# Kernel optimization log

Hardware: AMD Instinct MI355X
Metric: run time of the kernel (lower is better)

## Reference

```python
import jax, jax.numpy as jnp
import numpy as np

EPS = 1e-10


def setup_inputs() -> dict:
    key = jax.random.key(0)
    k1, k2 = jax.random.split(key)
    B, C, H, W = 8, 16, 256, 256
    x = jax.random.normal(k1, (B, C, H, W), dtype=jnp.float32)
    # grid_sample-style normalized coords in [-1, 1]
    inv_grid = jax.random.uniform(k2, (B, H, W, 2), dtype=jnp.float32, minval=-1.0, maxval=1.0)
    return {"x": x, "inv_grid": inv_grid}


def reference(x, inv_grid):
    B, C, Hin, Win = x.shape
    h, w = Hin, Win  # OH = OW = None -> output size equals input size

    g = (inv_grid + 1.0) * 0.5
    # coord 0 scaled by h, coord 1 by w, shifted by +1 (padding row/col), clamped
    ci = jnp.clip(g[..., 0] * h + 1.0, 0.0, h + 1 - 2 * EPS)
    cj = jnp.clip(g[..., 1] * w + 1.0, 0.0, w + 1 - 2 * EPS)
    i0 = jnp.floor(ci).astype(jnp.int32)  # coords >= 0 so floor == trunc (.long())
    j0 = jnp.floor(cj).astype(jnp.int32)

    # broadcast over channel dim (grid is shared across channels)
    ci_ = ci[:, None]
    cj_ = cj[:, None]
    i0_ = i0[:, None]
    j0_ = j0[:, None]

    bidx = jnp.arange(B)[:, None, None, None]
    cidx = jnp.arange(C)[None, :, None, None]

    A = jnp.zeros((B, C, h + 3, w + 3), dtype=x.dtype)
    for di in range(2):
        wi = jax.nn.relu(1.0 - jnp.abs(ci_ - (i0_ + di).astype(ci_.dtype)))
        for dj in range(2):
            wj = jax.nn.relu(1.0 - jnp.abs(cj_ - (j0_ + dj).astype(cj_.dtype)))
            # bilinear splat scatter-add of x * weight into the 4 corner cells
            A = A.at[bidx, cidx, i0_ + di, j0_ + dj].add(x * (wi * wj))
    return A[..., 1:h + 1, 1:w + 1]
```

## Files before the change

kernel.cpp:

```cpp
#include <hip/hip_runtime.h>
#include <hip/hip_fp16.h>
#include <stdint.h>

#define BB 8
#define CC 16
#define HH 256
#define WW 256
#define HW (HH * WW)
#define NSRC (BB * HW)
#define NBLK (NSRC / 256)
#define REC_DW 9
#define ELLCAP 12
#define MAXSLOT 15
#define CNT_BYTES ((size_t)NSRC * 4)


__global__ __launch_bounds__(256) void pass1_ell(
    const float* __restrict__ x,
    const float* __restrict__ inv_grid,
    uint32_t* __restrict__ counts,
    uint32_t* __restrict__ records)
{
    const int idx = blockIdx.x * 256 + threadIdx.x;
    const float2 g2 = ((const float2*)inv_grid)[idx];

    const float ci = fminf(fmaxf(fmaf((g2.x + 1.0f) * 0.5f, (float)HH, 1.0f), 0.0f), 257.0f);
    const float cj = fminf(fmaxf(fmaf((g2.y + 1.0f) * 0.5f, (float)WW, 1.0f), 0.0f), 257.0f);
    const int i0 = (int)floorf(ci);
    const int j0 = (int)floorf(cj);
    const float fi = ci - (float)i0;
    const float fj = cj - (float)j0;

    const int bi = i0 - 1, bj = j0 - 1;
    if (!(((unsigned)bi < HH) & ((unsigned)bj < WW))) return;

    const int b = idx >> 16;
    const int p = idx & 0xFFFF;

    const float* xp = x + (((size_t)b * CC) << 16) + p;
    float xv[CC];
#pragma unroll
    for (int q = 0; q < CC; ++q) xv[q] = xp[(size_t)q << 16];

    const uint32_t bin = (b << 16) | (bi << 8) | bj;
    const uint32_t slot = atomicAdd(&counts[bin], 1u);
    if (slot >= ELLCAP) return;

    uint32_t* rp = records + ((size_t)bin * ELLCAP + slot) * REC_DW;
    const uint32_t fi16 = (uint32_t)(fi * 65535.0f + 0.5f);
    const uint32_t fj16 = (uint32_t)(fj * 65535.0f + 0.5f);
    rp[0] = fi16 | (fj16 << 16);
#pragma unroll
    for (int q = 0; q < 8; ++q) {
        const uint32_t h0 = (uint32_t)__half_as_ushort(__float2half_rn(xv[2 * q]));
        const uint32_t h1 = (uint32_t)__half_as_ushort(__float2half_rn(xv[2 * q + 1]));
        rp[1 + q] = h0 | (h1 << 16);
    }
}

__global__ __launch_bounds__(256) void gather_ell(
    const uint32_t* __restrict__ counts,
    const uint32_t* __restrict__ records,
    float* __restrict__ out)
{
    const int g   = blockIdx.x;
    const int b   = g & 7;
    const int seq = g >> 3;
    const int r   = ((seq >> 4) << 4) + (threadIdx.x >> 4);
    const int c   = ((seq & 15) << 4) + (threadIdx.x & 15);

    float acc[CC];
#pragma unroll
    for (int q = 0; q < CC; ++q) acc[q] = 0.0f;

#pragma unroll
    for (int di = 0; di < 2; ++di) {
        const int i0c = r + di;
        if (i0c < 1) continue;
#pragma unroll
        for (int dj = 0; dj < 2; ++dj) {
            const int j0c = c + dj;
            if (j0c < 1) continue;
            const uint32_t bin = (b << 16) | ((i0c - 1) << 8) | (j0c - 1);
            uint32_t cnt = counts[bin];
            if (cnt > ELLCAP) cnt = ELLCAP;
            const uint32_t* rp = records + (size_t)bin * (ELLCAP * REC_DW);
            for (uint32_t k = 0; k < cnt; ++k, rp += REC_DW) {
                const uint32_t ff = rp[0];
                const float fi = (float)(ff & 0xFFFFu) * (1.0f / 65535.0f);
                const float fj = (float)(ff >> 16)     * (1.0f / 65535.0f);
                const float wi = di ? (1.0f - fi) : fi;
                const float wj = dj ? (1.0f - fj) : fj;
                const float w = wi * wj;
#pragma unroll
                for (int q = 0; q < 8; ++q) {
                    const uint32_t u = rp[1 + q];
                    const float v0 = __half2float(__ushort_as_half((unsigned short)(u & 0xFFFFu)));
                    const float v1 = __half2float(__ushort_as_half((unsigned short)(u >> 16)));
                    acc[2 * q]     += w * v0;
                    acc[2 * q + 1] += w * v1;
                }
            }
        }
    }

    float* op = out + (((size_t)(b * CC)) << 16) + (r << 8) + c;
#pragma unroll
    for (int q = 0; q < CC; ++q)
        op[(size_t)q << 16] = acc[q];
}

__global__ __launch_bounds__(256) void pass1_bin(
    const float* __restrict__ inv_grid,
    uint32_t* __restrict__ counts,
    uint32_t* __restrict__ srcmeta,
    uint32_t* __restrict__ fifj)
{
    const int idx = blockIdx.x * 256 + threadIdx.x;
    const float2 g2 = ((const float2*)inv_grid)[idx];
    const float ci = fminf(fmaxf(fmaf((g2.x + 1.0f) * 0.5f, (float)HH, 1.0f), 0.0f), 257.0f);
    const float cj = fminf(fmaxf(fmaf((g2.y + 1.0f) * 0.5f, (float)WW, 1.0f), 0.0f), 257.0f);
    const int i0 = (int)floorf(ci);
    const int j0 = (int)floorf(cj);
    const float fi = ci - (float)i0;
    const float fj = cj - (float)j0;
    const int bi = i0 - 1, bj = j0 - 1;
    uint32_t meta = 0xFFFFFFFFu;
    if (((unsigned)bi < HH) & ((unsigned)bj < WW)) {
        const int b = idx >> 16;
        const uint32_t bin = (b << 16) | (bi << 8) | bj;
        const uint32_t slot = atomicAdd(&counts[bin], 1u);
        if (slot < MAXSLOT) meta = (bin << 4) | slot;
    }
    srcmeta[idx] = meta;
    const uint32_t fi16 = (uint32_t)(fi * 65535.0f + 0.5f);
    const uint32_t fj16 = (uint32_t)(fj * 65535.0f + 0.5f);
    fifj[idx] = fi16 | (fj16 << 16);
}

__global__ __launch_bounds__(256) void scanA(
    const uint32_t* __restrict__ counts,
    uint32_t* __restrict__ offsets,
    uint32_t* __restrict__ bsum)
{
    __shared__ uint32_t s[256];
    const int t = threadIdx.x;
    const int i = blockIdx.x * 256 + t;
    const uint32_t v = counts[i];
    s[t] = v;
    __syncthreads();
#pragma unroll
    for (int d = 1; d < 256; d <<= 1) {
        const uint32_t u = (t >= d) ? s[t - d] : 0u;
        __syncthreads();
        s[t] += u;
        __syncthreads();
    }
    offsets[i] = s[t] - v;
    if (t == 255) bsum[blockIdx.x] = s[255];
}

__global__ __launch_bounds__(1024) void scanB(uint32_t* __restrict__ bsum)
{
    __shared__ uint32_t s[1024];
    const int t = threadIdx.x;
    const uint32_t a  = bsum[2 * t];
    const uint32_t b2 = bsum[2 * t + 1];
    const uint32_t pair = a + b2;
    s[t] = pair;
    __syncthreads();
#pragma unroll
    for (int d = 1; d < 1024; d <<= 1) {
        const uint32_t u = (t >= d) ? s[t - d] : 0u;
        __syncthreads();
        s[t] += u;
        __syncthreads();
    }
    const uint32_t excl = s[t] - pair;
    bsum[2 * t]     = excl;
    bsum[2 * t + 1] = excl + a;
}

__global__ __launch_bounds__(256) void fill_records(
    const float* __restrict__ x,
    const uint32_t* __restrict__ srcmeta,
    const uint32_t* __restrict__ fifj,
    const uint32_t* __restrict__ offsets,
    const uint32_t* __restrict__ bsum,
    uint32_t* __restrict__ records)
{
    const int idx = blockIdx.x * 256 + threadIdx.x;
    const uint32_t meta = srcmeta[idx];
    if (meta == 0xFFFFFFFFu) return;
    const uint32_t bin  = meta >> 4;
    const uint32_t slot = meta & 15u;
    const uint32_t pos  = offsets[bin] + bsum[bin >> 8] + slot;
    const int b = idx >> 16;
    const int p = idx & 0xFFFF;
    const float* xp = x + (((size_t)b * CC) << 16) + p;
    uint32_t* rp = records + (size_t)pos * REC_DW;
    rp[0] = fifj[idx];
#pragma unroll
    for (int q = 0; q < 8; ++q) {
        const float v0 = xp[(size_t)(2 * q)     << 16];
        const float v1 = xp[(size_t)(2 * q + 1) << 16];
        const uint32_t h0 = (uint32_t)__half_as_ushort(__float2half_rn(v0));
        const uint32_t h1 = (uint32_t)__half_as_ushort(__float2half_rn(v1));
        rp[1 + q] = h0 | (h1 << 16);
    }
}

__global__ __launch_bounds__(256) void gather_csr(
    const uint32_t* __restrict__ counts,
    const uint32_t* __restrict__ offsets,
    const uint32_t* __restrict__ bsum,
    const uint32_t* __restrict__ records,
    float* __restrict__ out)
{
    const int g   = blockIdx.x;
    const int b   = g & 7;
    const int seq = g >> 3;
    const int r   = ((seq >> 4) << 4) + (threadIdx.x >> 4);
    const int c   = ((seq & 15) << 4) + (threadIdx.x & 15);

    float acc[CC];
#pragma unroll
    for (int q = 0; q < CC; ++q) acc[q] = 0.0f;

#pragma unroll
    for (int di = 0; di < 2; ++di) {
        const int i0c = r + di;
        if (i0c < 1) continue;
#pragma unroll
        for (int dj = 0; dj < 2; ++dj) {
            const int j0c = c + dj;
            if (j0c < 1) continue;
            const uint32_t bin = (b << 16) | ((i0c - 1) << 8) | (j0c - 1);
            uint32_t cnt = counts[bin];
            if (cnt > MAXSLOT) cnt = MAXSLOT;
            const uint32_t off = offsets[bin] + bsum[bin >> 8];
            const uint32_t* rp = records + (size_t)off * REC_DW;
            for (uint32_t k = 0; k < cnt; ++k, rp += REC_DW) {
                const uint32_t ff = rp[0];
                const float fi = (float)(ff & 0xFFFFu) * (1.0f / 65535.0f);
                const float fj = (float)(ff >> 16)     * (1.0f / 65535.0f);
                const float wi = di ? (1.0f - fi) : fi;
                const float wj = dj ? (1.0f - fj) : fj;
                const float w = wi * wj;
#pragma unroll
                for (int q = 0; q < 8; ++q) {
                    const uint32_t u = rp[1 + q];
                    const float v0 = __half2float(__ushort_as_half((unsigned short)(u & 0xFFFFu)));
                    const float v1 = __half2float(__ushort_as_half((unsigned short)(u >> 16)));
                    acc[2 * q]     += w * v0;
                    acc[2 * q + 1] += w * v1;
                }
            }
        }
    }

    float* op = out + (((size_t)(b * CC)) << 16) + (r << 8) + c;
#pragma unroll
    for (int q = 0; q < CC; ++q)
        op[(size_t)q << 16] = acc[q];
}

__global__ __launch_bounds__(256) void invgrid_scatter_direct(
    const float* __restrict__ x,
    const float* __restrict__ inv_grid,
    float* __restrict__ out)
{
    const int idx = blockIdx.x * 256 + threadIdx.x;
    const int b = idx >> 16;
    const float2 g2 = ((const float2*)inv_grid)[idx];
    const float ci = fminf(fmaxf(fmaf((g2.x + 1.0f) * 0.5f, (float)HH, 1.0f), 0.0f), 257.0f);
    const float cj = fminf(fmaxf(fmaf((g2.y + 1.0f) * 0.5f, (float)WW, 1.0f), 0.0f), 257.0f);
    const int i0 = (int)floorf(ci);
    const int j0 = (int)floorf(cj);
    const float wi0 = fmaxf(0.0f, 1.0f - fabsf(ci - (float)i0));
    const float wi1 = fmaxf(0.0f, 1.0f - fabsf(ci - (float)(i0 + 1)));
    const float wj0 = fmaxf(0.0f, 1.0f - fabsf(cj - (float)j0));
    const float wj1 = fmaxf(0.0f, 1.0f - fabsf(cj - (float)(j0 + 1)));
    const float w00 = wi0 * wj0, w01 = wi0 * wj1;
    const float w10 = wi1 * wj0, w11 = wi1 * wj1;
    const int r0 = i0 - 1, r1 = i0, c0 = j0 - 1, c1 = j0;
    const bool vr0 = (unsigned)r0 < HH, vr1 = (unsigned)r1 < HH;
    const bool vc0 = (unsigned)c0 < WW, vc1 = (unsigned)c1 < WW;
    const int o00 = r0 * WW + c0, o01 = r0 * WW + c1;
    const int o10 = r1 * WW + c0, o11 = r1 * WW + c1;
    const int p = idx & 0xFFFF;
    const float* xp = x + (size_t)b * CC * HW + p;
    float* op = out + (size_t)b * CC * HW;
#pragma unroll
    for (int cch = 0; cch < CC; ++cch) {
        const float xv = xp[(size_t)cch * HW];
        float* ob = op + (size_t)cch * HW;
        if (vr0 & vc0) atomicAdd(ob + o00, xv * w00);
        if (vr0 & vc1) atomicAdd(ob + o01, xv * w01);
        if (vr1 & vc0) atomicAdd(ob + o10, xv * w10);
        if (vr1 & vc1) atomicAdd(ob + o11, xv * w11);
    }
}

extern "C" void kernel_launch(void* const* d_in, const int* in_sizes, int n_in,
                              void* d_out, int out_size, void* d_ws, size_t ws_size,
                              hipStream_t stream) {
    const float* x        = (const float*)d_in[0];
    const float* inv_grid = (const float*)d_in[1];
    float* out            = (float*)d_out;

    const size_t ell_need = CNT_BYTES + (size_t)NSRC * ELLCAP * REC_DW * 4;

    const size_t A = 256;
    size_t o_counts  = 0;
    size_t o_offsets = o_counts  + ((size_t)NSRC * 4 + A - 1) / A * A;
    size_t o_bsum    = o_offsets + ((size_t)NSRC * 4 + A - 1) / A * A;
    size_t o_srcmeta = o_bsum    + ((size_t)NBLK * 4 + A - 1) / A * A;
    size_t o_fifj    = o_srcmeta + ((size_t)NSRC * 4 + A - 1) / A * A;
    size_t o_records = o_fifj    + ((size_t)NSRC * 4 + A - 1) / A * A;
    size_t csr_need  = o_records + (size_t)NSRC * REC_DW * 4;

    if (ws_size >= ell_need) {
        uint32_t* counts  = (uint32_t*)d_ws;
        uint32_t* records = (uint32_t*)((char*)d_ws + CNT_BYTES);
        hipMemsetAsync(counts, 0, CNT_BYTES, stream);
        pass1_ell <<<NBLK, 256, 0, stream>>>(x, inv_grid, counts, records);
        gather_ell<<<NBLK, 256, 0, stream>>>(counts, records, out);
    } else if (ws_size >= csr_need) {
        char* w = (char*)d_ws;
        uint32_t* counts  = (uint32_t*)(w + o_counts);
        uint32_t* offsets = (uint32_t*)(w + o_offsets);
        uint32_t* bsum    = (uint32_t*)(w + o_bsum);
        uint32_t* srcmeta = (uint32_t*)(w + o_srcmeta);
        uint32_t* fifj    = (uint32_t*)(w + o_fifj);
        uint32_t* records = (uint32_t*)(w + o_records);
        hipMemsetAsync(counts, 0, (size_t)NSRC * 4, stream);
        pass1_bin   <<<NBLK, 256,  0, stream>>>(inv_grid, counts, srcmeta, fifj);
        scanA       <<<NBLK, 256,  0, stream>>>(counts, offsets, bsum);
        scanB       <<<1,    1024, 0, stream>>>(bsum);
        fill_records<<<NBLK, 256,  0, stream>>>(x, srcmeta, fifj, offsets, bsum, records);
        gather_csr  <<<NBLK, 256,  0, stream>>>(counts, offsets, bsum, records, out);
    } else {
        hipMemsetAsync(d_out, 0, (size_t)out_size * sizeof(float), stream);
        invgrid_scatter_direct<<<NBLK, 256, 0, stream>>>(x, inv_grid, out);
    }
}
```

Baseline: 165.3 us.

## Split ELL build into meta and fill passes with slot-major SoA records

Splits the first pass into a metadata kernel that does the atomic slot allocation and a separate fill kernel that reads x and writes fp16 payloads. Records move from an interleaved 9-dword layout to a slot-major structure-of-arrays: one array of packed weights and one of 32-byte payloads written as two uint4 stores. This is meant to give coalesced, vectorized stores in the fill step and coalesced loads in the gather, where neighbouring threads read neighbouring bins at the same slot. The cost is an extra kernel launch, an intermediate srcs buffer, and a larger workspace requirement. If the workspace is too small, execution falls back to the CSR path.

```diff
diff --git a/kernel.cpp b/kernel.cpp
--- a/kernel.cpp
+++ b/kernel.cpp
@@ -9,17 +9,16 @@
 #define HW (HH * WW)
 #define NSRC (BB * HW)
 #define NBLK (NSRC / 256)
-#define REC_DW 9
 #define ELLCAP 12
 #define MAXSLOT 15
+#define REC_DW 9
 #define CNT_BYTES ((size_t)NSRC * 4)
 
 
-__global__ __launch_bounds__(256) void pass1_ell(
-    const float* __restrict__ x,
+__global__ __launch_bounds__(256) void pass1_meta(
     const float* __restrict__ inv_grid,
     uint32_t* __restrict__ counts,
-    uint32_t* __restrict__ records)
+    uint2* __restrict__ srcs)
 {
     const int idx = blockIdx.x * 256 + threadIdx.x;
     const float2 g2 = ((const float2*)inv_grid)[idx];
@@ -32,35 +31,54 @@
     const float fj = cj - (float)j0;
 
     const int bi = i0 - 1, bj = j0 - 1;
-    if (!(((unsigned)bi < HH) & ((unsigned)bj < WW))) return;
+    uint32_t pos = 0xFFFFFFFFu;
+    if (((unsigned)bi < HH) & ((unsigned)bj < WW)) {
+        const int b = idx >> 16;
+        const uint32_t bin = (b << 16) | (bi << 8) | bj;
+        const uint32_t slot = atomicAdd(&counts[bin], 1u);
+        if (slot < ELLCAP) pos = slot * (uint32_t)NSRC + bin;
+    }
+    const uint32_t fi16 = (uint32_t)(fi * 65535.0f + 0.5f);
+    const uint32_t fj16 = (uint32_t)(fj * 65535.0f + 0.5f);
+    uint2 m; m.x = pos; m.y = fi16 | (fj16 << 16);
+    srcs[idx] = m;
+}
+
+__global__ __launch_bounds__(256) void fill_ell(
+    const float* __restrict__ x,
+    const uint2* __restrict__ srcs,
+    uint32_t* __restrict__ ff,
+    uint4* __restrict__ pl)
+{
+    const int idx = blockIdx.x * 256 + threadIdx.x;
+    const uint2 m = srcs[idx];
+    if (m.x == 0xFFFFFFFFu) return;
+    const uint32_t pos = m.x;
 
     const int b = idx >> 16;
     const int p = idx & 0xFFFF;
-
     const float* xp = x + (((size_t)b * CC) << 16) + p;
-    float xv[CC];
-#pragma unroll
-    for (int q = 0; q < CC; ++q) xv[q] = xp[(size_t)q << 16];
-
-    const uint32_t bin = (b << 16) | (bi << 8) | bj;
-    const uint32_t slot = atomicAdd(&counts[bin], 1u);
-    if (slot >= ELLCAP) return;
-
-    uint32_t* rp = records + ((size_t)bin * ELLCAP + slot) * REC_DW;
-    const uint32_t fi16 = (uint32_t)(fi * 65535.0f + 0.5f);
-    const uint32_t fj16 = (uint32_t)(fj * 65535.0f + 0.5f);
-    rp[0] = fi16 | (fj16 << 16);
+
+    uint32_t h[8];
 #pragma unroll
     for (int q = 0; q < 8; ++q) {
-        const uint32_t h0 = (uint32_t)__half_as_ushort(__float2half_rn(xv[2 * q]));
-        const uint32_t h1 = (uint32_t)__half_as_ushort(__float2half_rn(xv[2 * q + 1]));
-        rp[1 + q] = h0 | (h1 << 16);
-    }
+        const float v0 = xp[(size_t)(2 * q)     << 16];
+        const float v1 = xp[(size_t)(2 * q + 1) << 16];
+        const uint32_t h0 = (uint32_t)__half_as_ushort(__float2half_rn(v0));
+        const uint32_t h1 = (uint32_t)__half_as_ushort(__float2half_rn(v1));
+        h[q] = h0 | (h1 << 16);
+    }
+    ff[pos] = m.y;
+    uint4 q0; q0.x = h[0]; q0.y = h[1]; q0.z = h[2]; q0.w = h[3];
+    uint4 q1; q1.x = h[4]; q1.y = h[5]; q1.z = h[6]; q1.w = h[7];
+    pl[(size_t)pos * 2]     = q0;
+    pl[(size_t)pos * 2 + 1] = q1;
 }
 
 __global__ __launch_bounds__(256) void gather_ell(
     const uint32_t* __restrict__ counts,
-    const uint32_t* __restrict__ records,
+    const uint32_t* __restrict__ ff,
+    const uint4* __restrict__ pl,
     float* __restrict__ out)
 {
     const int g   = blockIdx.x;
@@ -84,19 +102,21 @@
             const uint32_t bin = (b << 16) | ((i0c - 1) << 8) | (j0c - 1);
             uint32_t cnt = counts[bin];
             if (cnt > ELLCAP) cnt = ELLCAP;
-            const uint32_t* rp = records + (size_t)bin * (ELLCAP * REC_DW);
-            for (uint32_t k = 0; k < cnt; ++k, rp += REC_DW) {
-                const uint32_t ff = rp[0];
-                const float fi = (float)(ff & 0xFFFFu) * (1.0f / 65535.0f);
-                const float fj = (float)(ff >> 16)     * (1.0f / 65535.0f);
+            for (uint32_t k = 0; k < cnt; ++k) {
+                const uint32_t pos = k * (uint32_t)NSRC + bin;
+                const uint32_t f2 = ff[pos];
+                const float fi = (float)(f2 & 0xFFFFu) * (1.0f / 65535.0f);
+                const float fj = (float)(f2 >> 16)     * (1.0f / 65535.0f);
                 const float wi = di ? (1.0f - fi) : fi;
                 const float wj = dj ? (1.0f - fj) : fj;
                 const float w = wi * wj;
+                const uint4 q0 = pl[(size_t)pos * 2];
+                const uint4 q1 = pl[(size_t)pos * 2 + 1];
+                const uint32_t hs[8] = {q0.x, q0.y, q0.z, q0.w, q1.x, q1.y, q1.z, q1.w};
 #pragma unroll
                 for (int q = 0; q < 8; ++q) {
-                    const uint32_t u = rp[1 + q];
-                    const float v0 = __half2float(__ushort_as_half((unsigned short)(u & 0xFFFFu)));
-                    const float v1 = __half2float(__ushort_as_half((unsigned short)(u >> 16)));
+                    const float v0 = __half2float(__ushort_as_half((unsigned short)(hs[q] & 0xFFFFu)));
+                    const float v1 = __half2float(__ushort_as_half((unsigned short)(hs[q] >> 16)));
                     acc[2 * q]     += w * v0;
                     acc[2 * q + 1] += w * v1;
                 }
@@ -241,9 +261,9 @@
             const uint32_t off = offsets[bin] + bsum[bin >> 8];
             const uint32_t* rp = records + (size_t)off * REC_DW;
             for (uint32_t k = 0; k < cnt; ++k, rp += REC_DW) {
-                const uint32_t ff = rp[0];
-                const float fi = (float)(ff & 0xFFFFu) * (1.0f / 65535.0f);
-                const float fj = (float)(ff >> 16)     * (1.0f / 65535.0f);
+                const uint32_t f2 = rp[0];
+                const float fi = (float)(f2 & 0xFFFFu) * (1.0f / 65535.0f);
+                const float fj = (float)(f2 >> 16)     * (1.0f / 65535.0f);
                 const float wi = di ? (1.0f - fi) : fi;
                 const float wj = dj ? (1.0f - fj) : fj;
                 const float w = wi * wj;
@@ -309,23 +329,31 @@
     const float* inv_grid = (const float*)d_in[1];
     float* out            = (float*)d_out;
 
-    const size_t ell_need = CNT_BYTES + (size_t)NSRC * ELLCAP * REC_DW * 4;
-
     const size_t A = 256;
+    size_t e_counts = 0;
+    size_t e_srcs   = e_counts + (CNT_BYTES + A - 1) / A * A;
+    size_t e_ff     = e_srcs   + ((size_t)NSRC * 8 + A - 1) / A * A;
+    size_t e_pl     = e_ff     + ((size_t)NSRC * ELLCAP * 4 + A - 1) / A * A;
+    size_t ell_need = e_pl     + (size_t)NSRC * ELLCAP * 32;
+
     size_t o_counts  = 0;
-    size_t o_offsets = o_counts  + ((size_t)NSRC * 4 + A - 1) / A * A;
-    size_t o_bsum    = o_offsets + ((size_t)NSRC * 4 + A - 1) / A * A;
+    size_t o_offsets = o_counts  + (CNT_BYTES + A - 1) / A * A;
+    size_t o_bsum    = o_offsets + (CNT_BYTES + A - 1) / A * A;
     size_t o_srcmeta = o_bsum    + ((size_t)NBLK * 4 + A - 1) / A * A;
-    size_t o_fifj    = o_srcmeta + ((size_t)NSRC * 4 + A - 1) / A * A;
-    size_t o_records = o_fifj    + ((size_t)NSRC * 4 + A - 1) / A * A;
+    size_t o_fifj    = o_srcmeta + (CNT_BYTES + A - 1) / A * A;
+    size_t o_records = o_fifj    + (CNT_BYTES + A - 1) / A * A;
     size_t csr_need  = o_records + (size_t)NSRC * REC_DW * 4;
 
     if (ws_size >= ell_need) {
-        uint32_t* counts  = (uint32_t*)d_ws;
-        uint32_t* records = (uint32_t*)((char*)d_ws + CNT_BYTES);
+        char* w = (char*)d_ws;
+        uint32_t* counts = (uint32_t*)(w + e_counts);
+        uint2*    srcs   = (uint2*)   (w + e_srcs);
+        uint32_t* ff     = (uint32_t*)(w + e_ff);
+        uint4*    pl     = (uint4*)   (w + e_pl);
         hipMemsetAsync(counts, 0, CNT_BYTES, stream);
-        pass1_ell <<<NBLK, 256, 0, stream>>>(x, inv_grid, counts, records);
-        gather_ell<<<NBLK, 256, 0, stream>>>(counts, records, out);
+        pass1_meta<<<NBLK, 256, 0, stream>>>(inv_grid, counts, srcs);
+        fill_ell  <<<NBLK, 256, 0, stream>>>(x, srcs, ff, pl);
+        gather_ell<<<NBLK, 256, 0, stream>>>(counts, ff, pl, out);
     } else if (ws_size >= csr_need) {
         char* w = (char*)d_ws;
         uint32_t* counts  = (uint32_t*)(w + o_counts);
@@ -334,7 +362,7 @@
         uint32_t* srcmeta = (uint32_t*)(w + o_srcmeta);
         uint32_t* fifj    = (uint32_t*)(w + o_fifj);
         uint32_t* records = (uint32_t*)(w + o_records);
-        hipMemsetAsync(counts, 0, (size_t)NSRC * 4, stream);
+        hipMemsetAsync(counts, 0, CNT_BYTES, stream);
         pass1_bin   <<<NBLK, 256,  0, stream>>>(inv_grid, counts, srcmeta, fifj);
         scanA       <<<NBLK, 256,  0, stream>>>(counts, offsets, bsum);
         scanB       <<<1,    1024, 0, stream>>>(bsum);
```

Result: faster. 161.6 us (-2.3%).
